# Kernel optimization log

Measured on AMD Instinct MI355X. Metric: run time of the kernel, lower is better.

## Reference

```python
import jax, jax.numpy as jnp
import numpy as np

B, SEQ, IN, H = 256, 128, 512, 512


def setup_inputs() -> dict:
    key = jax.random.key(0)
    ks = jax.random.split(key, 7)
    s = 1.0 / np.sqrt(H)  # torch LSTM/Linear default init scale
    return {
        "x": jax.random.normal(ks[0], (B, SEQ, IN), dtype=jnp.float32),
        "W_ih": jax.random.uniform(ks[1], (4 * H, IN), jnp.float32, -s, s),
        "W_hh": jax.random.uniform(ks[2], (4 * H, H), jnp.float32, -s, s),
        "b_ih": jax.random.uniform(ks[3], (4 * H,), jnp.float32, -s, s),
        "b_hh": jax.random.uniform(ks[4], (4 * H,), jnp.float32, -s, s),
        "Wa": jax.random.uniform(ks[5], (SEQ, H), jnp.float32, -s, s),
        "ba": jax.random.uniform(ks[6], (SEQ,), jnp.float32, -s, s),
    }


def _lstm_cell(xi, h, c, W_ih, W_hh, b):
    # torch gate order: input, forget, cell(g), output
    gates = xi @ W_ih.T + h @ W_hh.T + b  # [B, 4H]
    i, f, g, o = jnp.split(gates, 4, axis=-1)
    c_new = jax.nn.sigmoid(f) * c + jax.nn.sigmoid(i) * jnp.tanh(g)
    h_new = jax.nn.sigmoid(o) * jnp.tanh(c_new)
    return h_new, c_new


def reference(x, W_ih, W_hh, b_ih, b_hh, Wa, ba):
    b = b_ih + b_hh
    bs, seq = x.shape[0], Wa.shape[0]
    h = jnp.zeros((bs, W_hh.shape[1]), x.dtype)
    c = jnp.zeros_like(h)
    # initial step on zero input (x[:,0]*0), zero initial state
    h, c = _lstm_cell(jnp.zeros((bs, x.shape[2]), x.dtype), h, c, W_ih, W_hh, b)

    def step(carry, _):
        h, c = carry
        attn = jax.nn.softmax(c @ Wa.T + ba, axis=-1)      # [B, seq]
        xi = jnp.einsum('bs,bsd->bd', attn, x)             # attention-weighted input
        h, c = _lstm_cell(xi, h, c, W_ih, W_hh, b)
        return (h, c), h

    _, hs = jax.lax.scan(step, (h, c), None, length=seq)   # [seq, B, H]
    return jnp.transpose(hs, (1, 0, 2))                    # [B, seq, H]
```

## Files before the change

### kernel.cpp

```cpp
#include <hip/hip_runtime.h>
#include <stdint.h>

#define BDIM 256
#define SEQL 128
#define IND 512
#define HID 512
#define KDIM 1024

typedef __bf16 bf16x8 __attribute__((ext_vector_type(8)));
typedef float floatx4 __attribute__((ext_vector_type(4)));
typedef _Float16 f16x8 __attribute__((ext_vector_type(8)));

__device__ __forceinline__ float sigm(float x) { return 1.0f / (1.0f + __expf(-x)); }

__device__ __forceinline__ ushort f2bf(float v) {
  uint32_t x = __builtin_bit_cast(uint32_t, v);
  x += 0x7fffu + ((x >> 16) & 1u);
  return (ushort)(x >> 16);
}
__device__ __forceinline__ float bf2f(ushort u) {
  return __builtin_bit_cast(float, ((uint32_t)u) << 16);
}

__global__ __launch_bounds__(256) void k_wconv(
    const float* __restrict__ W_ih, const float* __restrict__ W_hh,
    const float* __restrict__ b_ih, const float* __restrict__ b_hh,
    ushort* __restrict__ Whi, ushort* __restrict__ Wlo, float* __restrict__ bias) {
  int row = blockIdx.x;
  if (threadIdx.x == 0) bias[row] = b_ih[row] + b_hh[row];
  for (int k = threadIdx.x; k < KDIM; k += 256) {
    float w = (k < IND) ? W_ih[(size_t)row * IND + k] : W_hh[(size_t)row * HID + (k - IND)];
    ushort hi = f2bf(w);
    Whi[(size_t)row * KDIM + k] = hi;
    Wlo[(size_t)row * KDIM + k] = f2bf(w - bf2f(hi));
  }
}

__global__ __launch_bounds__(256) void k_xconv(const float* __restrict__ x,
                                               _Float16* __restrict__ xh) {
  size_t i = ((size_t)blockIdx.x * 256 + threadIdx.x) * 8;
  float4 v0 = *(const float4*)(x + i);
  float4 v1 = *(const float4*)(x + i + 4);
  f16x8 o;
  o[0] = (_Float16)v0.x; o[1] = (_Float16)v0.y; o[2] = (_Float16)v0.z; o[3] = (_Float16)v0.w;
  o[4] = (_Float16)v1.x; o[5] = (_Float16)v1.y; o[6] = (_Float16)v1.z; o[7] = (_Float16)v1.w;
  *(f16x8*)(xh + i) = o;
}

__global__ void k_init(const float* __restrict__ b_ih, const float* __restrict__ b_hh,
                       float* __restrict__ c, ushort* __restrict__ Ahi, ushort* __restrict__ Alo) {
  int b = blockIdx.x;
  for (int j = threadIdx.x; j < HID; j += blockDim.x) {
    float bi = b_ih[j] + b_hh[j];
    float bg = b_ih[2 * HID + j] + b_hh[2 * HID + j];
    float bo = b_ih[3 * HID + j] + b_hh[3 * HID + j];
    float c0 = sigm(bi) * tanhf(bg);
    float h0 = sigm(bo) * tanhf(c0);
    c[b * HID + j] = c0;
    ushort hi = f2bf(h0);
    Ahi[(size_t)b * KDIM + IND + j] = hi;
    Alo[(size_t)b * KDIM + IND + j] = f2bf(h0 - bf2f(hi));
  }
}

struct AttnS { float sc[HID]; float sl[SEQL]; float sxi[4][HID]; };
struct GemmS {
  ushort sA[2][2][16][72];
  ushort sW[2][2][64][72];
  float  sR[4][16][16];
};
union SU { AttnS a; GemmS g; };

#define G3LOAD(R, KO) do { \
  R##a  = *(const uint4*)(gA + (KO)); \
  R##w0 = *(const uint4*)(gWhi + (KO));      R##w1 = *(const uint4*)(gWhi + (KO) + 8);  \
  R##w2 = *(const uint4*)(gWlo + (KO));      R##w3 = *(const uint4*)(gWlo + (KO) + 8);  } while (0)
#define G3STORE(BUF, R) do { \
  *(uint4*)&su.g.sA[BUF][sthalf][ar][ac] = R##a; \
  *(uint4*)&su.g.sW[BUF][0][wr][wc] = R##w0;  *(uint4*)&su.g.sW[BUF][0][wr][wc + 8] = R##w1; \
  *(uint4*)&su.g.sW[BUF][1][wr][wc] = R##w2;  *(uint4*)&su.g.sW[BUF][1][wr][wc + 8] = R##w3; } while (0)
#define G3COMPUTE(BUF) do { \
  _Pragma("unroll") for (int ks = 0; ks < 2; ++ks) { \
    int kb = ks * 32 + koff; \
    bf16x8 ah = *(const bf16x8*)(&su.g.sA[BUF][0][ml][kb]); \
    bf16x8 al = *(const bf16x8*)(&su.g.sA[BUF][1][ml][kb]); \
    bf16x8 wh = *(const bf16x8*)(&su.g.sW[BUF][0][g * 16 + ml][kb]); \
    bf16x8 wl = *(const bf16x8*)(&su.g.sW[BUF][1][g * 16 + ml][kb]); \
    accA = __builtin_amdgcn_mfma_f32_16x16x32_bf16(ah, wh, accA, 0, 0, 0); \
    accB = __builtin_amdgcn_mfma_f32_16x16x32_bf16(ah, wl, accB, 0, 0, 0); \
    accB = __builtin_amdgcn_mfma_f32_16x16x32_bf16(al, wh, accB, 0, 0, 0); } } while (0)
#define G3LOOP(NCH) \
  G3LOAD(A, 0); G3LOAD(B, 64); \
  G3STORE(0, A); G3STORE(1, B); \
  G3LOAD(A, 128); G3LOAD(B, 192); \
  __syncthreads(); \
  for (int k0 = 0; k0 < (NCH); k0 += 2) { \
    G3COMPUTE(0); \
    __syncthreads(); \
    if (k0 + 2 < (NCH)) { G3STORE(0, A); if (k0 + 4 < (NCH)) G3LOAD(A, (k0 + 4) * 64); } \
    G3COMPUTE(1); \
    __syncthreads(); \
    if (k0 + 3 < (NCH)) { G3STORE(1, B); if (k0 + 5 < (NCH)) G3LOAD(B, (k0 + 5) * 64); } \
  }

__global__ __launch_bounds__(256) void k1_attn_gatesH(
    const float* __restrict__ c, const float* __restrict__ Wa,
    const float* __restrict__ ba, const _Float16* __restrict__ xh,
    const ushort* __restrict__ Whi, const ushort* __restrict__ Wlo,
    ushort* __restrict__ Rhi, ushort* __restrict__ Rlo,
    float* __restrict__ P) {
  __shared__ __align__(16) SU su;
  int blk = blockIdx.x, tid = threadIdx.x;
  int lane = tid & 63, wave = tid >> 6;

  if (blk < 256) {
    int b = blk;
    su.a.sc[tid] = c[b * HID + tid];
    su.a.sc[tid + 256] = c[b * HID + tid + 256];
    __syncthreads();
    float4 c0 = *(const float4*)(&su.a.sc[lane * 4]);
    float4 c1 = *(const float4*)(&su.a.sc[lane * 4 + 256]);
#pragma unroll 4
    for (int si = 0; si < 32; ++si) {
      int s = wave * 32 + si;
      const float4* wr4 = (const float4*)(Wa + (size_t)s * HID);
      float4 w0 = wr4[lane];
      float4 w1 = wr4[lane + 64];
      float acc = c0.x * w0.x + c0.y * w0.y + c0.z * w0.z + c0.w * w0.w
                + c1.x * w1.x + c1.y * w1.y + c1.z * w1.z + c1.w * w1.w;
#pragma unroll
      for (int off = 32; off > 0; off >>= 1) acc += __shfl_down(acc, off);
      if (lane == 0) su.a.sl[s] = acc + ba[s];
    }
    __syncthreads();
    if (tid < 64) {
      float v0 = su.a.sl[tid], v1 = su.a.sl[tid + 64];
      float m = fmaxf(v0, v1);
#pragma unroll
      for (int off = 32; off > 0; off >>= 1) m = fmaxf(m, __shfl_xor(m, off));
      float e0 = __expf(v0 - m), e1 = __expf(v1 - m);
      float s2 = e0 + e1;
#pragma unroll
      for (int off = 32; off > 0; off >>= 1) s2 += __shfl_xor(s2, off);
      float inv = 1.f / s2;
      su.a.sl[tid] = e0 * inv; su.a.sl[tid + 64] = e1 * inv;
    }
    __syncthreads();
    int cix = tid & 63, qp = tid >> 6;
    const _Float16* xrow = xh + (size_t)b * SEQL * IND + (size_t)qp * 32 * IND + 8 * cix;
    float a0 = 0.f, a1 = 0.f, a2 = 0.f, a3 = 0.f, a4 = 0.f, a5 = 0.f, a6 = 0.f, a7 = 0.f;
#pragma unroll 8
    for (int s = 0; s < 32; ++s) {
      float w = su.a.sl[qp * 32 + s];
      f16x8 v = *(const f16x8*)(xrow + (size_t)s * IND);
      a0 += w * (float)v[0]; a1 += w * (float)v[1];
      a2 += w * (float)v[2]; a3 += w * (float)v[3];
      a4 += w * (float)v[4]; a5 += w * (float)v[5];
      a6 += w * (float)v[6]; a7 += w * (float)v[7];
    }
    *(float4*)(&su.a.sxi[qp][8 * cix])     = (float4){a0, a1, a2, a3};
    *(float4*)(&su.a.sxi[qp][8 * cix + 4]) = (float4){a4, a5, a6, a7};
    __syncthreads();
    float rx = su.a.sxi[0][2 * tid] + su.a.sxi[1][2 * tid] + su.a.sxi[2][2 * tid] + su.a.sxi[3][2 * tid];
    float ry = su.a.sxi[0][2 * tid + 1] + su.a.sxi[1][2 * tid + 1] + su.a.sxi[2][2 * tid + 1] + su.a.sxi[3][2 * tid + 1];
    ushort hx = f2bf(rx), hy = f2bf(ry);
    uint hp = (uint)hx | ((uint)hy << 16);
    uint lp = (uint)f2bf(rx - bf2f(hx)) | ((uint)f2bf(ry - bf2f(hy)) << 16);
    *(uint*)(Rhi + (size_t)b * KDIM + 2 * tid) = hp;
    *(uint*)(Rlo + (size_t)b * KDIM + 2 * tid) = lp;
  } else {
    int g2 = blk - 256;
    int lb = (g2 & 7) * 64 + (g2 >> 3);
    int j0 = (lb >> 4) * 16;
    int b0 = (lb & 15) * 16;
    int sthalf = tid >> 7;
    int ar = (tid & 127) >> 3, ac = (tid & 7) * 8;
    const ushort* gA = (sthalf ? Rlo : Rhi) + (size_t)(b0 + ar) * KDIM + IND + ac;
    int wr = tid >> 2, wc = (tid & 3) * 16;
    int wrow = (wr >> 4) * HID + j0 + (wr & 15);
    const ushort* gWhi = Whi + (size_t)wrow * KDIM + IND + wc;
    const ushort* gWlo = Wlo + (size_t)wrow * KDIM + IND + wc;

    floatx4 accA = {0.f, 0.f, 0.f, 0.f}, accB = {0.f, 0.f, 0.f, 0.f};
    int g = tid >> 6, ml = lane & 15, koff = (lane >> 4) * 8;
    uint4 Aa, Aw0, Aw1, Aw2, Aw3, Ba, Bw0, Bw1, Bw2, Bw3;
    G3LOOP(8)

    floatx4 acc = accA + accB;
    size_t pbase = (((size_t)g * 32 + (j0 >> 4)) * 16 + (b0 >> 4)) * 256;
    *(float4*)(P + pbase + ml * 16 + (lane >> 4) * 4) = *(float4*)&acc;
  }
}

__global__ __launch_bounds__(256) void k2_gatesX(
    const ushort* __restrict__ Whi, const ushort* __restrict__ Wlo,
    const float* __restrict__ bias, const float* __restrict__ P,
    const ushort* __restrict__ Rhi, const ushort* __restrict__ Rlo,
    float* __restrict__ c, float* __restrict__ out,
    ushort* __restrict__ Dhi, ushort* __restrict__ Dlo, int tstep) {
  __shared__ __align__(16) SU su;
  int bid = blockIdx.x, tid = threadIdx.x;
  int lane = tid & 63;
  int lb = (bid & 7) * 64 + (bid >> 3);
  int j0 = (lb >> 4) * 16;
  int b0 = (lb & 15) * 16;
  int sthalf = tid >> 7;
  int ar = (tid & 127) >> 3, ac = (tid & 7) * 8;
  const ushort* gA = (sthalf ? Rlo : Rhi) + (size_t)(b0 + ar) * KDIM + ac;
  int wr = tid >> 2, wc = (tid & 3) * 16;
  int wrow = (wr >> 4) * HID + j0 + (wr & 15);
  const ushort* gWhi = Whi + (size_t)wrow * KDIM + wc;
  const ushort* gWlo = Wlo + (size_t)wrow * KDIM + wc;

  floatx4 accA = {0.f, 0.f, 0.f, 0.f}, accB = {0.f, 0.f, 0.f, 0.f};
  int g = tid >> 6, ml = lane & 15, koff = (lane >> 4) * 8;
  uint4 Aa, Aw0, Aw1, Aw2, Aw3, Ba, Bw0, Bw1, Bw2, Bw3;
  G3LOOP(8)

  {
    floatx4 acc = accA + accB;
#pragma unroll
    for (int r = 0; r < 4; ++r) su.g.sR[g][ml][(lane >> 4) * 4 + r] = acc[r];
  }
  __syncthreads();

  {
    int jj = tid & 15, bb = tid >> 4;
    int jg = j0 + jj;
    int b = b0 + bb;
    size_t pb = (((size_t)(j0 >> 4)) * 16 + (b0 >> 4)) * 256 + jj * 16 + bb;
    const size_t gstr = (size_t)32 * 16 * 256;
    float ig = sigm(su.g.sR[0][jj][bb] + P[pb]            + bias[jg]);
    float fg = sigm(su.g.sR[1][jj][bb] + P[pb + gstr]     + bias[HID + jg]);
    float gg = tanhf(su.g.sR[2][jj][bb] + P[pb + 2 * gstr] + bias[2 * HID + jg]);
    float og = sigm(su.g.sR[3][jj][bb] + P[pb + 3 * gstr] + bias[3 * HID + jg]);
    float co = c[b * HID + jg];
    float cn = fg * co + ig * gg;
    float hv = og * tanhf(cn);
    c[b * HID + jg] = cn;
    out[((size_t)b * SEQL + tstep) * HID + jg] = hv;
    ushort hi = f2bf(hv);
    Dhi[(size_t)b * KDIM + IND + jg] = hi;
    Dlo[(size_t)b * KDIM + IND + jg] = f2bf(hv - bf2f(hi));
  }
}

extern "C" void kernel_launch(void* const* d_in, const int* in_sizes, int n_in,
                              void* d_out, int out_size, void* d_ws, size_t ws_size,
                              hipStream_t stream) {
  (void)in_sizes; (void)n_in; (void)out_size; (void)ws_size;
  const float* x    = (const float*)d_in[0];
  const float* W_ih = (const float*)d_in[1];
  const float* W_hh = (const float*)d_in[2];
  const float* b_ih = (const float*)d_in[3];
  const float* b_hh = (const float*)d_in[4];
  const float* Wa   = (const float*)d_in[5];
  const float* ba   = (const float*)d_in[6];
  float* out = (float*)d_out;

  char* p = (char*)d_ws;
  auto carve = [&](size_t bytes) { char* r = p; p += (bytes + 255) & ~(size_t)255; return r; };
  float*  c    = (float*)carve((size_t)BDIM * HID * 4);
  float*  bias = (float*)carve((size_t)4 * HID * 4);
  ushort* Whi  = (ushort*)carve((size_t)4 * HID * KDIM * 2);
  ushort* Wlo  = (ushort*)carve((size_t)4 * HID * KDIM * 2);
  ushort* A0hi = (ushort*)carve((size_t)BDIM * KDIM * 2);
  ushort* A0lo = (ushort*)carve((size_t)BDIM * KDIM * 2);
  ushort* A1hi = (ushort*)carve((size_t)BDIM * KDIM * 2);
  ushort* A1lo = (ushort*)carve((size_t)BDIM * KDIM * 2);
  _Float16* xh = (_Float16*)carve((size_t)BDIM * SEQL * IND * 2);
  float*  P    = (float*)carve((size_t)4 * HID * BDIM * 4);

  k_wconv<<<4 * HID, 256, 0, stream>>>(W_ih, W_hh, b_ih, b_hh, Whi, Wlo, bias);
  k_xconv<<<(BDIM * SEQL * IND) / (256 * 8), 256, 0, stream>>>(x, xh);
  k_init<<<BDIM, 256, 0, stream>>>(b_ih, b_hh, c, A0hi, A0lo);

  for (int t = 0; t < SEQL; ++t) {
    ushort* Rhi = (t & 1) ? A1hi : A0hi;
    ushort* Rlo = (t & 1) ? A1lo : A0lo;
    ushort* Dhi = (t & 1) ? A0hi : A1hi;
    ushort* Dlo = (t & 1) ? A0lo : A1lo;
    k1_attn_gatesH<<<768, 256, 0, stream>>>(c, Wa, ba, xh, Whi, Wlo, Rhi, Rlo, P);
    k2_gatesX<<<512, 256, 0, stream>>>(Whi, Wlo, bias, P, Rhi, Rlo, c, out, Dhi, Dlo, t);
  }
}
```

Before: 4.385 ms.

## Fuse attention and both gate GEMMs into one per-step kernel with flag sync

The two per-timestep kernels become one launch. Attention blocks write the attention-weighted input and then bump a per-batch-tile atomic counter. GEMM blocks first compute the h-part of the gates, spin-wait on that counter, then accumulate the x-part and apply the LSTM cell, which removes the P scratch round trip and one launch per step. This relies on all 768 blocks being co-resident, or on attention blocks being scheduled before the waiting GEMM blocks, to avoid deadlock. Spin-waiting blocks also occupy CUs.

```diff
diff --git a/kernel.cpp b/kernel.cpp
--- a/kernel.cpp
+++ b/kernel.cpp
@@ -63,7 +63,7 @@
   }
 }
 
-struct AttnS { float sc[HID]; float sl[SEQL]; float sxi[4][HID]; };
+struct AttnS { float sl[SEQL]; float sxi[4][HID]; };
 struct GemmS {
   ushort sA[2][2][16][72];
   ushort sW[2][2][64][72];
@@ -103,34 +103,34 @@
     if (k0 + 3 < (NCH)) { G3STORE(1, B); if (k0 + 5 < (NCH)) G3LOAD(B, (k0 + 5) * 64); } \
   }
 
-__global__ __launch_bounds__(256) void k1_attn_gatesH(
-    const float* __restrict__ c, const float* __restrict__ Wa,
+__global__ __launch_bounds__(256) void k_step(
+    float* __restrict__ c, const float* __restrict__ Wa,
     const float* __restrict__ ba, const _Float16* __restrict__ xh,
     const ushort* __restrict__ Whi, const ushort* __restrict__ Wlo,
+    const float* __restrict__ bias,
     ushort* __restrict__ Rhi, ushort* __restrict__ Rlo,
-    float* __restrict__ P) {
+    ushort* __restrict__ Dhi, ushort* __restrict__ Dlo,
+    float* __restrict__ out, unsigned* __restrict__ flag, int t) {
   __shared__ __align__(16) SU su;
   int blk = blockIdx.x, tid = threadIdx.x;
   int lane = tid & 63, wave = tid >> 6;
-
-  if (blk < 256) {
-    int b = blk;
-    su.a.sc[tid] = c[b * HID + tid];
-    su.a.sc[tid + 256] = c[b * HID + tid + 256];
-    __syncthreads();
-    float4 c0 = *(const float4*)(&su.a.sc[lane * 4]);
-    float4 c1 = *(const float4*)(&su.a.sc[lane * 4 + 256]);
+  int n = blk & 7, s = blk >> 3;
+
+  if (s < 32) {
+    int b = s * 8 + n;
+    float4 c0 = *(const float4*)(c + (size_t)b * HID + lane * 4);
+    float4 c1 = *(const float4*)(c + (size_t)b * HID + lane * 4 + 256);
 #pragma unroll 4
     for (int si = 0; si < 32; ++si) {
-      int s = wave * 32 + si;
-      const float4* wr4 = (const float4*)(Wa + (size_t)s * HID);
+      int ss = wave * 32 + si;
+      const float4* wr4 = (const float4*)(Wa + (size_t)ss * HID);
       float4 w0 = wr4[lane];
       float4 w1 = wr4[lane + 64];
       float acc = c0.x * w0.x + c0.y * w0.y + c0.z * w0.z + c0.w * w0.w
                 + c1.x * w1.x + c1.y * w1.y + c1.z * w1.z + c1.w * w1.w;
 #pragma unroll
       for (int off = 32; off > 0; off >>= 1) acc += __shfl_down(acc, off);
-      if (lane == 0) su.a.sl[s] = acc + ba[s];
+      if (lane == 0) su.a.sl[ss] = acc + ba[ss];
     }
     __syncthreads();
     if (tid < 64) {
@@ -150,9 +150,9 @@
     const _Float16* xrow = xh + (size_t)b * SEQL * IND + (size_t)qp * 32 * IND + 8 * cix;
     float a0 = 0.f, a1 = 0.f, a2 = 0.f, a3 = 0.f, a4 = 0.f, a5 = 0.f, a6 = 0.f, a7 = 0.f;
 #pragma unroll 8
-    for (int s = 0; s < 32; ++s) {
-      float w = su.a.sl[qp * 32 + s];
-      f16x8 v = *(const f16x8*)(xrow + (size_t)s * IND);
+    for (int ss = 0; ss < 32; ++ss) {
+      float w = su.a.sl[qp * 32 + ss];
+      f16x8 v = *(const f16x8*)(xrow + (size_t)ss * IND);
       a0 += w * (float)v[0]; a1 += w * (float)v[1];
       a2 += w * (float)v[2]; a3 += w * (float)v[3];
       a4 += w * (float)v[4]; a5 += w * (float)v[5];
@@ -168,80 +168,63 @@
     uint lp = (uint)f2bf(rx - bf2f(hx)) | ((uint)f2bf(ry - bf2f(hy)) << 16);
     *(uint*)(Rhi + (size_t)b * KDIM + 2 * tid) = hp;
     *(uint*)(Rlo + (size_t)b * KDIM + 2 * tid) = lp;
+    __syncthreads();
+    if (tid == 0)
+      __hip_atomic_fetch_add(flag + (b >> 4) * 16, 1u, __ATOMIC_RELEASE, __HIP_MEMORY_SCOPE_AGENT);
   } else {
-    int g2 = blk - 256;
-    int lb = (g2 & 7) * 64 + (g2 >> 3);
-    int j0 = (lb >> 4) * 16;
-    int b0 = (lb & 15) * 16;
+    int q = s - 32;
+    int jt = 4 * n + (q & 3);
+    int bt = q >> 2;
+    int j0 = jt * 16, b0 = bt * 16;
     int sthalf = tid >> 7;
     int ar = (tid & 127) >> 3, ac = (tid & 7) * 8;
-    const ushort* gA = (sthalf ? Rlo : Rhi) + (size_t)(b0 + ar) * KDIM + IND + ac;
     int wr = tid >> 2, wc = (tid & 3) * 16;
+    int g = tid >> 6, ml = lane & 15, koff = (lane >> 4) * 8;
     int wrow = (wr >> 4) * HID + j0 + (wr & 15);
+
+    floatx4 accA = {0.f, 0.f, 0.f, 0.f}, accB = {0.f, 0.f, 0.f, 0.f};
+    uint4 Aa, Aw0, Aw1, Aw2, Aw3, Ba, Bw0, Bw1, Bw2, Bw3;
+
+    const ushort* gA  = (sthalf ? Rlo : Rhi) + (size_t)(b0 + ar) * KDIM + IND + ac;
     const ushort* gWhi = Whi + (size_t)wrow * KDIM + IND + wc;
     const ushort* gWlo = Wlo + (size_t)wrow * KDIM + IND + wc;
-
-    floatx4 accA = {0.f, 0.f, 0.f, 0.f}, accB = {0.f, 0.f, 0.f, 0.f};
-    int g = tid >> 6, ml = lane & 15, koff = (lane >> 4) * 8;
-    uint4 Aa, Aw0, Aw1, Aw2, Aw3, Ba, Bw0, Bw1, Bw2, Bw3;
     G3LOOP(8)
 
-    floatx4 acc = accA + accB;
-    size_t pbase = (((size_t)g * 32 + (j0 >> 4)) * 16 + (b0 >> 4)) * 256;
-    *(float4*)(P + pbase + ml * 16 + (lane >> 4) * 4) = *(float4*)&acc;
-  }
-}
-
-__global__ __launch_bounds__(256) void k2_gatesX(
-    const ushort* __restrict__ Whi, const ushort* __restrict__ Wlo,
-    const float* __restrict__ bias, const float* __restrict__ P,
-    const ushort* __restrict__ Rhi, const ushort* __restrict__ Rlo,
-    float* __restrict__ c, float* __restrict__ out,
-    ushort* __restrict__ Dhi, ushort* __restrict__ Dlo, int tstep) {
-  __shared__ __align__(16) SU su;
-  int bid = blockIdx.x, tid = threadIdx.x;
-  int lane = tid & 63;
-  int lb = (bid & 7) * 64 + (bid >> 3);
-  int j0 = (lb >> 4) * 16;
-  int b0 = (lb & 15) * 16;
-  int sthalf = tid >> 7;
-  int ar = (tid & 127) >> 3, ac = (tid & 7) * 8;
-  const ushort* gA = (sthalf ? Rlo : Rhi) + (size_t)(b0 + ar) * KDIM + ac;
-  int wr = tid >> 2, wc = (tid & 3) * 16;
-  int wrow = (wr >> 4) * HID + j0 + (wr & 15);
-  const ushort* gWhi = Whi + (size_t)wrow * KDIM + wc;
-  const ushort* gWlo = Wlo + (size_t)wrow * KDIM + wc;
-
-  floatx4 accA = {0.f, 0.f, 0.f, 0.f}, accB = {0.f, 0.f, 0.f, 0.f};
-  int g = tid >> 6, ml = lane & 15, koff = (lane >> 4) * 8;
-  uint4 Aa, Aw0, Aw1, Aw2, Aw3, Ba, Bw0, Bw1, Bw2, Bw3;
-  G3LOOP(8)
-
-  {
-    floatx4 acc = accA + accB;
-#pragma unroll
-    for (int r = 0; r < 4; ++r) su.g.sR[g][ml][(lane >> 4) * 4 + r] = acc[r];
-  }
-  __syncthreads();
-
-  {
-    int jj = tid & 15, bb = tid >> 4;
-    int jg = j0 + jj;
-    int b = b0 + bb;
-    size_t pb = (((size_t)(j0 >> 4)) * 16 + (b0 >> 4)) * 256 + jj * 16 + bb;
-    const size_t gstr = (size_t)32 * 16 * 256;
-    float ig = sigm(su.g.sR[0][jj][bb] + P[pb]            + bias[jg]);
-    float fg = sigm(su.g.sR[1][jj][bb] + P[pb + gstr]     + bias[HID + jg]);
-    float gg = tanhf(su.g.sR[2][jj][bb] + P[pb + 2 * gstr] + bias[2 * HID + jg]);
-    float og = sigm(su.g.sR[3][jj][bb] + P[pb + 3 * gstr] + bias[3 * HID + jg]);
-    float co = c[b * HID + jg];
-    float cn = fg * co + ig * gg;
-    float hv = og * tanhf(cn);
-    c[b * HID + jg] = cn;
-    out[((size_t)b * SEQL + tstep) * HID + jg] = hv;
-    ushort hi = f2bf(hv);
-    Dhi[(size_t)b * KDIM + IND + jg] = hi;
-    Dlo[(size_t)b * KDIM + IND + jg] = f2bf(hv - bf2f(hi));
+    if (tid == 0) {
+      while (__hip_atomic_load(flag + bt * 16, __ATOMIC_RELAXED, __HIP_MEMORY_SCOPE_AGENT)
+             < 16u * (unsigned)(t + 1))
+        __builtin_amdgcn_s_sleep(2);
+      (void)__hip_atomic_load(flag + bt * 16, __ATOMIC_ACQUIRE, __HIP_MEMORY_SCOPE_AGENT);
+    }
+    __syncthreads();
+
+    gA  = (sthalf ? Rlo : Rhi) + (size_t)(b0 + ar) * KDIM + ac;
+    gWhi = Whi + (size_t)wrow * KDIM + wc;
+    gWlo = Wlo + (size_t)wrow * KDIM + wc;
+    G3LOOP(8)
+
+    {
+      floatx4 acc = accA + accB;
+#pragma unroll
+      for (int r = 0; r < 4; ++r) su.g.sR[g][ml][(lane >> 4) * 4 + r] = acc[r];
+    }
+    __syncthreads();
+    {
+      int jj = tid & 15, bb = tid >> 4;
+      int jg = j0 + jj, b = b0 + bb;
+      float ig = sigm(su.g.sR[0][jj][bb] + bias[jg]);
+      float fg = sigm(su.g.sR[1][jj][bb] + bias[HID + jg]);
+      float gg = tanhf(su.g.sR[2][jj][bb] + bias[2 * HID + jg]);
+      float og = sigm(su.g.sR[3][jj][bb] + bias[3 * HID + jg]);
+      float co = c[(size_t)b * HID + jg];
+      float cn = fg * co + ig * gg;
+      float hv = og * tanhf(cn);
+      c[(size_t)b * HID + jg] = cn;
+      out[((size_t)b * SEQL + t) * HID + jg] = hv;
+      ushort hi = f2bf(hv);
+      Dhi[(size_t)b * KDIM + IND + jg] = hi;
+      Dlo[(size_t)b * KDIM + IND + jg] = f2bf(hv - bf2f(hi));
+    }
   }
 }
 
@@ -260,6 +243,7 @@
 
   char* p = (char*)d_ws;
   auto carve = [&](size_t bytes) { char* r = p; p += (bytes + 255) & ~(size_t)255; return r; };
+  unsigned* flag = (unsigned*)carve(1024);
   float*  c    = (float*)carve((size_t)BDIM * HID * 4);
   float*  bias = (float*)carve((size_t)4 * HID * 4);
   ushort* Whi  = (ushort*)carve((size_t)4 * HID * KDIM * 2);
@@ -269,8 +253,8 @@
   ushort* A1hi = (ushort*)carve((size_t)BDIM * KDIM * 2);
   ushort* A1lo = (ushort*)carve((size_t)BDIM * KDIM * 2);
   _Float16* xh = (_Float16*)carve((size_t)BDIM * SEQL * IND * 2);
-  float*  P    = (float*)carve((size_t)4 * HID * BDIM * 4);
-
+
+  hipMemsetAsync(flag, 0, 1024, stream);
   k_wconv<<<4 * HID, 256, 0, stream>>>(W_ih, W_hh, b_ih, b_hh, Whi, Wlo, bias);
   k_xconv<<<(BDIM * SEQL * IND) / (256 * 8), 256, 0, stream>>>(x, xh);
   k_init<<<BDIM, 256, 0, stream>>>(b_ih, b_hh, c, A0hi, A0lo);
@@ -280,7 +264,7 @@
     ushort* Rlo = (t & 1) ? A1lo : A0lo;
     ushort* Dhi = (t & 1) ? A0hi : A1hi;
     ushort* Dlo = (t & 1) ? A0lo : A1lo;
-    k1_attn_gatesH<<<768, 256, 0, stream>>>(c, Wa, ba, xh, Whi, Wlo, Rhi, Rlo, P);
-    k2_gatesX<<<512, 256, 0, stream>>>(Whi, Wlo, bias, P, Rhi, Rlo, c, out, Dhi, Dlo, t);
-  }
-}
+    k_step<<<768, 256, 0, stream>>>(c, Wa, ba, xh, Whi, Wlo, bias,
+                                    Rhi, Rlo, Dhi, Dlo, out, flag, t);
+  }
+}
```

Result: slower. 5.262 ms (+20.0%).
